# Performance work log

Measured on AMD Instinct MI355X. Metric: run time of the kernel, lower is better.

The kernel has to match this reference:

```python
import jax, jax.numpy as jnp
import numpy as np

N_NODES = 100000
N_EDGES = 1600000
IN_CH = 128
HID = 64
N_CLASSES = 16
N_GRAPHS = 64


def setup_inputs() -> dict:
    key = jax.random.key(0)
    ks = jax.random.split(key, 10)
    x = jax.random.normal(ks[0], (N_NODES, IN_CH), dtype=jnp.float32)
    edge_index = jax.random.randint(ks[1], (2, N_EDGES), 0, N_NODES, dtype=jnp.int64)
    edge_weight = jax.random.uniform(ks[2], (N_EDGES,), dtype=jnp.float32)
    batch = jnp.sort(jax.random.randint(ks[3], (N_NODES,), 0, N_GRAPHS, dtype=jnp.int64))
    s1 = 1.0 / np.sqrt(IN_CH)
    s2 = 1.0 / np.sqrt(HID)
    W1 = jax.random.uniform(ks[4], (IN_CH, HID), jnp.float32, -s1, s1)
    b1 = jnp.zeros((HID,), jnp.float32)
    W2 = jax.random.uniform(ks[5], (HID, HID), jnp.float32, -s2, s2)
    b2 = jnp.zeros((HID,), jnp.float32)
    Wl = jax.random.uniform(ks[6], (HID, N_CLASSES), jnp.float32, -s2, s2)
    bl = jax.random.uniform(ks[7], (N_CLASSES,), jnp.float32, -s2, s2)
    return {"x": x, "edge_index": edge_index, "edge_weight": edge_weight,
            "batch": batch, "W1": W1, "b1": b1, "W2": W2, "b2": b2,
            "Wl": Wl, "bl": bl}


def _gcn_conv(x, src, dst, ew, W, b, n_nodes):
    # PyG GCNConv: h = x @ W; symmetric normalization with self-loops;
    # out[dst] += norm * h[src]; out += bias.
    deg = jax.ops.segment_sum(ew, dst, num_segments=n_nodes)
    deg_inv_sqrt = jnp.where(deg > 0, jax.lax.rsqrt(jnp.maximum(deg, 1e-30)), 0.0)
    norm = deg_inv_sqrt[src] * ew * deg_inv_sqrt[dst]  # [E']
    h = x @ W                                          # [N, out]
    msg = h[src] * norm[:, None]                       # [E', out] gather
    out = jax.ops.segment_sum(msg, dst, num_segments=n_nodes)  # scatter-add
    return out + b


def reference(x, edge_index, edge_weight, batch, W1, b1, W2, b2, Wl, bl):
    n = x.shape[0]
    # add self loops once (weight 1.0), shared by both conv layers
    loop = jnp.arange(n, dtype=edge_index.dtype)
    src = jnp.concatenate([edge_index[0], loop])
    dst = jnp.concatenate([edge_index[1], loop])
    ew = jnp.concatenate([edge_weight, jnp.ones((n,), edge_weight.dtype)])

    h = jax.nn.relu(_gcn_conv(x, src, dst, ew, W1, b1, n))
    h = jax.nn.relu(_gcn_conv(h, src, dst, ew, W2, b2, n))

    # global_mean_pool over graphs
    sums = jax.ops.segment_sum(h, batch, num_segments=N_GRAPHS)  # [G, HID]
    cnt = jax.ops.segment_sum(jnp.ones((n,), h.dtype), batch, num_segments=N_GRAPHS)
    pooled = sums / jnp.maximum(cnt, 1.0)[:, None]

    return pooled @ Wl + bl
```

## Files before the change

### kernel.cpp

```cpp
#include <hip/hip_runtime.h>
#include <hip/hip_fp16.h>

#define N_NODES   100000
#define N_EDGES   1600000
#define IN_CH     128
#define HID       64
#define N_CLASSES 16
#define N_GRAPHS  64

#define BK_SH     9
#define BK_NODES  512
#define NB        ((N_NODES + BK_NODES - 1) / BK_NODES)
#define BK_CAP    10240
#define CH_EDGES  4096
#define EPT       16
#define NCH       ((N_EDGES + CH_EDGES - 1) / CH_EDGES)
#define AGG_NPW   8

typedef __attribute__((ext_vector_type(8))) short bf16x8;
typedef __attribute__((ext_vector_type(4))) float f32x4;

__device__ __forceinline__ unsigned short f2bf(float f) {
    unsigned u = __float_as_uint(f);
    u += 0x7fffu + ((u >> 16) & 1u);
    return (unsigned short)(u >> 16);
}
__device__ __forceinline__ float4 bf4(uint2 v) {
    float4 o;
    o.x = __uint_as_float(v.x << 16);
    o.y = __uint_as_float(v.x & 0xffff0000u);
    o.z = __uint_as_float(v.y << 16);
    o.w = __uint_as_float(v.y & 0xffff0000u);
    return o;
}
__device__ __forceinline__ float dec_ew(unsigned v) {
    return __half2float(__ushort_as_half((unsigned short)(v >> 17)));
}

__global__ void k_init(int* __restrict__ bcursor, float* __restrict__ pooled,
                       float* __restrict__ cnt) {
    int i = blockIdx.x * 256 + threadIdx.x;
    if (i < NB) bcursor[i] = i * BK_CAP;
    if (i < N_GRAPHS * HID) pooled[i] = 0.0f;
    if (i < N_GRAPHS) cnt[i] = 0.0f;
}

__global__ void k_binscatter(const int* __restrict__ src, const int* __restrict__ dst,
                             const float* __restrict__ ew, int* __restrict__ bcursor,
                             int2* __restrict__ bedges) {
    __shared__ int  hist[NB];
    __shared__ int  offs[NB];
    __shared__ int  gbase[NB];
    __shared__ int  sc[256];
    __shared__ int2 stage[CH_EDGES];
    __shared__ int  dest[CH_EDGES];
    const int t = threadIdx.x;
    const int base = blockIdx.x * CH_EDGES;
    const int nloc = min(CH_EDGES, N_EDGES - base);

    for (int i = t; i < NB; i += 256) hist[i] = 0;
    __syncthreads();

    int myb[EPT], myr[EPT], myp[EPT]; float myw[EPT];
#pragma unroll
    for (int j = 0; j < EPT; ++j) {
        int i = base + j * 256 + t;
        if (i < N_EDGES) {
            int s = src[i], d = dst[i];
            int b = d >> BK_SH;
            myb[j] = b;
            myr[j] = atomicAdd(&hist[b], 1);
            myp[j] = s | ((d & (BK_NODES - 1)) << 17);
            myw[j] = ew[i];
        } else {
            myb[j] = -1;
        }
    }
    __syncthreads();

    int v = (t < NB) ? hist[t] : 0;
    sc[t] = v;
    __syncthreads();
    for (int off = 1; off < 256; off <<= 1) {
        int a = (t >= off) ? sc[t - off] : 0;
        __syncthreads();
        sc[t] += a;
        __syncthreads();
    }
    if (t < NB) {
        offs[t] = sc[t] - v;
        gbase[t] = (v > 0) ? atomicAdd(&bcursor[t], v) : 0;
    }
    __syncthreads();

#pragma unroll
    for (int j = 0; j < EPT; ++j) {
        if (myb[j] >= 0) {
            int p = offs[myb[j]] + myr[j];
            stage[p] = make_int2(myp[j], __float_as_int(myw[j]));
            dest[p] = gbase[myb[j]] + myr[j];
        }
    }
    __syncthreads();

    for (int i = t; i < nloc; i += 256)
        bedges[dest[i]] = stage[i];
}

__global__ __launch_bounds__(256) void k_build(const int* __restrict__ bcursor,
                                               const int2* __restrict__ bedges,
                                               int2* __restrict__ rowse,
                                               float* __restrict__ dis,
                                               unsigned* __restrict__ csr) {
    __shared__ int2  eds[BK_CAP];
    __shared__ int   cnt[BK_NODES];
    __shared__ float dsum[BK_NODES];
    __shared__ int   cur[BK_NODES];
    __shared__ int   sc[256];
    const int b = blockIdx.x;
    const int t = threadIdx.x;
    const int beg = b * BK_CAP, end = bcursor[b];
    const int n = end - beg;

    for (int i = t; i < BK_NODES; i += 256) { cnt[i] = 0; dsum[i] = 0.0f; }
    __syncthreads();

    for (int i = t; i < n; i += 256) {
        int2 e = bedges[beg + i];
        eds[i] = e;
        int dl = ((unsigned)e.x) >> 17;
        atomicAdd(&cnt[dl], 1);
        atomicAdd(&dsum[dl], __int_as_float(e.y));
    }
    __syncthreads();

    int a0 = cnt[2 * t], a1 = cnt[2 * t + 1];
    int pair = a0 + a1;
    sc[t] = pair;
    __syncthreads();
    for (int off = 1; off < 256; off <<= 1) {
        int a = (t >= off) ? sc[t - off] : 0;
        __syncthreads();
        sc[t] += a;
        __syncthreads();
    }
    int excl = sc[t] - pair;
    cur[2 * t] = excl;
    cur[2 * t + 1] = excl + a0;
    {
        int n0 = b * BK_NODES + 2 * t;
        if (n0 < N_NODES) {
            rowse[n0] = make_int2(beg + excl, beg + excl + a0);
            dis[n0] = rsqrtf(1.0f + dsum[2 * t]);
        }
        int n1 = n0 + 1;
        if (n1 < N_NODES) {
            rowse[n1] = make_int2(beg + excl + a0, beg + excl + a0 + a1);
            dis[n1] = rsqrtf(1.0f + dsum[2 * t + 1]);
        }
    }
    __syncthreads();

    for (int i = t; i < n; i += 256) {
        int2 e = eds[i];
        int dl = ((unsigned)e.x) >> 17;
        int s = e.x & 0x1FFFF;
        unsigned short w16 = __half_as_ushort(__float2half(__int_as_float(e.y)));
        int pos = beg + atomicAdd(&cur[dl], 1);
        csr[pos] = (unsigned)s | ((unsigned)w16 << 17);
    }
}

template <int K>
__global__ __launch_bounds__(256) void k_gemm(const float* __restrict__ x,
                                              const float* __restrict__ W,
                                              const float* __restrict__ dis,
                                              unsigned short* __restrict__ hb) {
    constexpr int AS = K + 8;
    __shared__ unsigned short a_s[64 * AS];
    __shared__ unsigned short wt[64 * AS];
    const int t    = threadIdx.x;
    const int lane = t & 63;
    const int wave = t >> 6;
    const int m    = lane & 15;
    const int quad = lane >> 4;
    const int rowbase = blockIdx.x * 64;

    constexpr int CPR = K / 8;
    for (int c = t; c < 64 * CPR; c += 256) {
        int row = c / CPR, cc = c % CPR;
        int gr = rowbase + row;
        float4 v0, v1;
        if (gr < N_NODES) {
            v0 = *(const float4*)&x[(long)gr * K + cc * 8];
            v1 = *(const float4*)&x[(long)gr * K + cc * 8 + 4];
        } else {
            v0 = make_float4(0.f, 0.f, 0.f, 0.f); v1 = v0;
        }
        uint4 p;
        p.x = f2bf(v0.x) | ((unsigned)f2bf(v0.y) << 16);
        p.y = f2bf(v0.z) | ((unsigned)f2bf(v0.w) << 16);
        p.z = f2bf(v1.x) | ((unsigned)f2bf(v1.y) << 16);
        p.w = f2bf(v1.z) | ((unsigned)f2bf(v1.w) << 16);
        *(uint4*)&a_s[row * AS + cc * 8] = p;
    }
    for (int idx = t; idx < K * 64; idx += 256) {
        int k = idx >> 6, n = idx & 63;
        wt[n * AS + k] = f2bf(W[idx]);
    }
    __syncthreads();

    bf16x8 bfrag[4][K / 32];
#pragma unroll
    for (int nt = 0; nt < 4; ++nt)
#pragma unroll
        for (int ks = 0; ks < K / 32; ++ks)
            bfrag[nt][ks] = *(const bf16x8*)&wt[(nt * 16 + m) * AS + ks * 32 + quad * 8];

    f32x4 acc[4];
#pragma unroll
    for (int nt = 0; nt < 4; ++nt) acc[nt] = (f32x4){0.f, 0.f, 0.f, 0.f};

#pragma unroll
    for (int ks = 0; ks < K / 32; ++ks) {
        bf16x8 af = *(const bf16x8*)&a_s[(wave * 16 + m) * AS + ks * 32 + quad * 8];
#pragma unroll
        for (int nt = 0; nt < 4; ++nt)
            acc[nt] = __builtin_amdgcn_mfma_f32_16x16x32_bf16(af, bfrag[nt][ks],
                                                              acc[nt], 0, 0, 0);
    }

#pragma unroll
    for (int i = 0; i < 4; ++i) {
        int gr = rowbase + wave * 16 + quad * 4 + i;
        if (gr < N_NODES) {
            float dsc = dis[gr];
#pragma unroll
            for (int nt = 0; nt < 4; ++nt)
                hb[(long)gr * HID + nt * 16 + m] = f2bf(dsc * acc[nt][i]);
        }
    }
}

__global__ void k_aggregate(const int2* __restrict__ rowse, const unsigned* __restrict__ csr,
                            const uint2* __restrict__ hb, const float* __restrict__ dis,
                            const float* __restrict__ b, float4* __restrict__ out4) {
    const int tid  = threadIdx.x;
    const int lane = tid & 63;
    const int g    = lane >> 4;
    const int c4   = lane & 15;
    const int nodebase = (blockIdx.x * 4 + (tid >> 6)) * AGG_NPW;
    const float4 bb = ((const float4*)b)[c4];

    if (nodebase >= N_NODES) return;

    int2 rs = rowse[nodebase];
    uint2 hsr = hb[nodebase * 16 + c4];

    for (int j = 0; j < AGG_NPW; ++j) {
        const int node = nodebase + j;
        if (node >= N_NODES) return;

        const int2 rs_c = rs;
        const float4 hs = bf4(hsr);
        if (j + 1 < AGG_NPW && node + 1 < N_NODES) {
            rs  = rowse[node + 1];
            hsr = hb[(node + 1) * 16 + c4];
        }

        float4 acc;
        if (g == 0) { acc = hs; }
        else        { acc.x = 0.f; acc.y = 0.f; acc.z = 0.f; acc.w = 0.f; }

        int p = rs_c.x;
        const int end = rs_c.y;

        unsigned d0, d1, d2, d3;
        if (p + 16 <= end) {
            d0 = csr[p + g];     d1 = csr[p + 4 + g];
            d2 = csr[p + 8 + g]; d3 = csr[p + 12 + g];
        }
        while (p + 16 <= end) {
            const unsigned e0 = d0, e1 = d1, e2 = d2, e3 = d3;
            const int pn = p + 16;
            if (pn + 16 <= end) {
                d0 = csr[pn + g];     d1 = csr[pn + 4 + g];
                d2 = csr[pn + 8 + g]; d3 = csr[pn + 12 + g];
            }
            float4 v0 = bf4(hb[(e0 & 0x1FFFF) * 16 + c4]);
            float4 v1 = bf4(hb[(e1 & 0x1FFFF) * 16 + c4]);
            float4 v2 = bf4(hb[(e2 & 0x1FFFF) * 16 + c4]);
            float4 v3 = bf4(hb[(e3 & 0x1FFFF) * 16 + c4]);
            float w0 = dec_ew(e0), w1 = dec_ew(e1);
            float w2 = dec_ew(e2), w3 = dec_ew(e3);
            acc.x += w0 * v0.x; acc.y += w0 * v0.y; acc.z += w0 * v0.z; acc.w += w0 * v0.w;
            acc.x += w1 * v1.x; acc.y += w1 * v1.y; acc.z += w1 * v1.z; acc.w += w1 * v1.w;
            acc.x += w2 * v2.x; acc.y += w2 * v2.y; acc.z += w2 * v2.z; acc.w += w2 * v2.w;
            acc.x += w3 * v3.x; acc.y += w3 * v3.y; acc.z += w3 * v3.z; acc.w += w3 * v3.w;
            p = pn;
        }
        if (p < end) {
            int i0 = p + g, i1 = p + 4 + g, i2 = p + 8 + g, i3 = p + 12 + g;
            unsigned e0 = csr[min(i0, end - 1)];
            unsigned e1 = csr[min(i1, end - 1)];
            unsigned e2 = csr[min(i2, end - 1)];
            unsigned e3 = csr[min(i3, end - 1)];
            float4 v0 = bf4(hb[(e0 & 0x1FFFF) * 16 + c4]);
            float4 v1 = bf4(hb[(e1 & 0x1FFFF) * 16 + c4]);
            float4 v2 = bf4(hb[(e2 & 0x1FFFF) * 16 + c4]);
            float4 v3 = bf4(hb[(e3 & 0x1FFFF) * 16 + c4]);
            float w0 = (i0 < end) ? dec_ew(e0) : 0.0f;
            float w1 = (i1 < end) ? dec_ew(e1) : 0.0f;
            float w2 = (i2 < end) ? dec_ew(e2) : 0.0f;
            float w3 = (i3 < end) ? dec_ew(e3) : 0.0f;
            acc.x += w0 * v0.x; acc.y += w0 * v0.y; acc.z += w0 * v0.z; acc.w += w0 * v0.w;
            acc.x += w1 * v1.x; acc.y += w1 * v1.y; acc.z += w1 * v1.z; acc.w += w1 * v1.w;
            acc.x += w2 * v2.x; acc.y += w2 * v2.y; acc.z += w2 * v2.z; acc.w += w2 * v2.w;
            acc.x += w3 * v3.x; acc.y += w3 * v3.y; acc.z += w3 * v3.z; acc.w += w3 * v3.w;
        }

        acc.x += __shfl_xor(acc.x, 16); acc.y += __shfl_xor(acc.y, 16);
        acc.z += __shfl_xor(acc.z, 16); acc.w += __shfl_xor(acc.w, 16);
        acc.x += __shfl_xor(acc.x, 32); acc.y += __shfl_xor(acc.y, 32);
        acc.z += __shfl_xor(acc.z, 32); acc.w += __shfl_xor(acc.w, 32);

        if (g == 0) {
            const float dd = dis[node];
            float4 o;
            o.x = fmaxf(dd * acc.x + bb.x, 0.0f);
            o.y = fmaxf(dd * acc.y + bb.y, 0.0f);
            o.z = fmaxf(dd * acc.z + bb.z, 0.0f);
            o.w = fmaxf(dd * acc.w + bb.w, 0.0f);
            out4[node * 16 + c4] = o;
        }
    }
}

#define POOL_NPB 256
__global__ __launch_bounds__(1024) void k_pool(const float* __restrict__ agg,
                                               const int* __restrict__ batch,
                                               float* __restrict__ pooled,
                                               float* __restrict__ cnt) {
    __shared__ float psh[N_GRAPHS * HID];
    __shared__ float csh[N_GRAPHS];
    const int tid = threadIdx.x;
    const int c = tid & 63;
    const int w = tid >> 6;
    const int nodebase = blockIdx.x * POOL_NPB + w * 16;

    for (int i = tid; i < N_GRAPHS * HID; i += 1024) psh[i] = 0.f;
    if (tid < N_GRAPHS) csh[tid] = 0.f;
    __syncthreads();

    int curg = -1; float accv = 0.f, cntacc = 0.f;
    for (int j = 0; j < 16; ++j) {
        int node = nodebase + j;
        if (node >= N_NODES) break;
        int g = batch[node];
        float v = agg[node * HID + c];
        if (g != curg) {
            if (curg >= 0) {
                atomicAdd(&psh[curg * HID + c], accv);
                if (c == 0) atomicAdd(&csh[curg], cntacc);
            }
            curg = g; accv = 0.f; cntacc = 0.f;
        }
        accv += v; cntacc += 1.f;
    }
    if (curg >= 0) {
        atomicAdd(&psh[curg * HID + c], accv);
        if (c == 0) atomicAdd(&csh[curg], cntacc);
    }
    __syncthreads();

    for (int i = tid; i < N_GRAPHS * HID; i += 1024) {
        if (csh[i >> 6] > 0.f) atomicAdd(&pooled[i], psh[i]);
    }
    if (tid < N_GRAPHS && csh[tid] > 0.f) atomicAdd(&cnt[tid], csh[tid]);
}

__global__ void k_out(const float* __restrict__ pooled, const float* __restrict__ cnt,
                      const float* __restrict__ Wl, const float* __restrict__ bl,
                      float* __restrict__ out) {
    int tid = threadIdx.x;
    int g = tid >> 4, k = tid & 15;
    float inv = 1.0f / fmaxf(cnt[g], 1.0f);
    float acc = 0.f;
#pragma unroll
    for (int h = 0; h < HID; ++h) acc += pooled[g * HID + h] * Wl[h * N_CLASSES + k];
    out[g * N_CLASSES + k] = acc * inv + bl[k];
}

extern "C" void kernel_launch(void* const* d_in, const int* in_sizes, int n_in,
                              void* d_out, int out_size, void* d_ws, size_t ws_size,
                              hipStream_t stream) {
    const float* x     = (const float*)d_in[0];
    const int*   ei    = (const int*)d_in[1];
    const float* ew    = (const float*)d_in[2];
    const int*   batch = (const int*)d_in[3];
    const float* W1    = (const float*)d_in[4];
    const float* b1    = (const float*)d_in[5];
    const float* W2    = (const float*)d_in[6];
    const float* b2    = (const float*)d_in[7];
    const float* Wl    = (const float*)d_in[8];
    const float* bl    = (const float*)d_in[9];

    const int* srcv = ei;
    const int* dstv = ei + N_EDGES;

    char* wsb = (char*)d_ws;
    float*          dis    = (float*)wsb;              wsb += 100352 * 4;
    int2*           rowse  = (int2*)wsb;               wsb += 100352 * 8;
    int*            bcursor= (int*)wsb;                wsb += 256 * 4;
    unsigned*       csr    = (unsigned*)wsb;           wsb += (size_t)NB * BK_CAP * 4;
    unsigned short* hb     = (unsigned short*)wsb;     wsb += N_NODES * HID * 2;
    float*          agg    = (float*)wsb;              wsb += N_NODES * HID * 4;
    float*          pooled = (float*)wsb;              wsb += N_GRAPHS * HID * 4;
    float*          cnt    = (float*)wsb;              wsb += N_GRAPHS * 4;
    float*          out    = (float*)d_out;
    int2*           bedges = (int2*)agg;

    k_init<<<16, 256, 0, stream>>>(bcursor, pooled, cnt);
    k_binscatter<<<NCH, 256, 0, stream>>>(srcv, dstv, ew, bcursor, bedges);
    k_build<<<NB, 256, 0, stream>>>(bcursor, bedges, rowse, dis, csr);

    const int agg_blocks = (N_NODES + 4 * AGG_NPW - 1) / (4 * AGG_NPW);

    k_gemm<IN_CH><<<(N_NODES + 63) / 64, 256, 0, stream>>>(x, W1, dis, hb);
    k_aggregate<<<agg_blocks, 256, 0, stream>>>(rowse, csr, (const uint2*)hb,
                                                dis, b1, (float4*)agg);
    k_gemm<HID><<<(N_NODES + 63) / 64, 256, 0, stream>>>(agg, W2, dis, hb);
    k_aggregate<<<agg_blocks, 256, 0, stream>>>(rowse, csr, (const uint2*)hb,
                                                dis, b2, (float4*)agg);

    k_pool<<<(N_NODES + POOL_NPB - 1) / POOL_NPB, 1024, 0, stream>>>(
        agg, batch, pooled, cnt);
    k_out<<<1, N_GRAPHS * N_CLASSES, 0, stream>>>(pooled, cnt, Wl, bl, out);
}
```

Measured before the change: 269.8 us.

## Simplify binscatter to direct writes and pass layer-1 output as bf16

The edge binning kernel drops the shared-memory prefix scan and staging buffer. It now uses smaller chunks with higher occupancy and writes each edge straight to its global bucket slot. The first aggregation now emits bf16 activations, and a new bf16-input GEMM reads them, halving intermediate traffic between layer 1 and layer 2. In exchange, the scatter writes are less coalesced, there are twice as many bcursor atomics, and rounding layer-1 outputs to bf16 adds precision loss.

```diff
diff --git a/kernel.cpp b/kernel.cpp
--- a/kernel.cpp
+++ b/kernel.cpp
@@ -12,8 +12,8 @@
 #define BK_NODES  512
 #define NB        ((N_NODES + BK_NODES - 1) / BK_NODES)
 #define BK_CAP    10240
-#define CH_EDGES  4096
-#define EPT       16
+#define CH_EDGES  2048
+#define EPT       8
 #define NCH       ((N_EDGES + CH_EDGES - 1) / CH_EDGES)
 #define AGG_NPW   8
 
@@ -45,18 +45,14 @@
     if (i < N_GRAPHS) cnt[i] = 0.0f;
 }
 
-__global__ void k_binscatter(const int* __restrict__ src, const int* __restrict__ dst,
-                             const float* __restrict__ ew, int* __restrict__ bcursor,
-                             int2* __restrict__ bedges) {
-    __shared__ int  hist[NB];
-    __shared__ int  offs[NB];
-    __shared__ int  gbase[NB];
-    __shared__ int  sc[256];
-    __shared__ int2 stage[CH_EDGES];
-    __shared__ int  dest[CH_EDGES];
+__global__ __launch_bounds__(256, 8) void k_binscatter(
+        const int* __restrict__ src, const int* __restrict__ dst,
+        const float* __restrict__ ew, int* __restrict__ bcursor,
+        int2* __restrict__ bedges) {
+    __shared__ int hist[NB];
+    __shared__ int gbase[NB];
     const int t = threadIdx.x;
     const int base = blockIdx.x * CH_EDGES;
-    const int nloc = min(CH_EDGES, N_EDGES - base);
 
     for (int i = t; i < NB; i += 256) hist[i] = 0;
     __syncthreads();
@@ -78,33 +74,18 @@
     }
     __syncthreads();
 
-    int v = (t < NB) ? hist[t] : 0;
-    sc[t] = v;
-    __syncthreads();
-    for (int off = 1; off < 256; off <<= 1) {
-        int a = (t >= off) ? sc[t - off] : 0;
-        __syncthreads();
-        sc[t] += a;
-        __syncthreads();
-    }
     if (t < NB) {
-        offs[t] = sc[t] - v;
+        int v = hist[t];
         gbase[t] = (v > 0) ? atomicAdd(&bcursor[t], v) : 0;
     }
     __syncthreads();
 
 #pragma unroll
     for (int j = 0; j < EPT; ++j) {
-        if (myb[j] >= 0) {
-            int p = offs[myb[j]] + myr[j];
-            stage[p] = make_int2(myp[j], __float_as_int(myw[j]));
-            dest[p] = gbase[myb[j]] + myr[j];
-        }
-    }
-    __syncthreads();
-
-    for (int i = t; i < nloc; i += 256)
-        bedges[dest[i]] = stage[i];
+        if (myb[j] >= 0)
+            bedges[gbase[myb[j]] + myr[j]] =
+                make_int2(myp[j], __float_as_int(myw[j]));
+    }
 }
 
 __global__ __launch_bounds__(256) void k_build(const int* __restrict__ bcursor,
@@ -242,9 +223,71 @@
     }
 }
 
+__global__ __launch_bounds__(256) void k_gemm2(const unsigned short* __restrict__ xb,
+                                               const float* __restrict__ W,
+                                               const float* __restrict__ dis,
+                                               unsigned short* __restrict__ hb) {
+    constexpr int K = HID;
+    constexpr int AS = K + 8;
+    __shared__ unsigned short a_s[64 * AS];
+    __shared__ unsigned short wt[64 * AS];
+    const int t    = threadIdx.x;
+    const int lane = t & 63;
+    const int wave = t >> 6;
+    const int m    = lane & 15;
+    const int quad = lane >> 4;
+    const int rowbase = blockIdx.x * 64;
+
+    for (int c = t; c < 64 * 8; c += 256) {
+        int row = c >> 3, cc = c & 7;
+        int gr = rowbase + row;
+        uint4 p = (gr < N_NODES) ? *(const uint4*)&xb[(long)gr * K + cc * 8]
+                                 : make_uint4(0, 0, 0, 0);
+        *(uint4*)&a_s[row * AS + cc * 8] = p;
+    }
+    for (int idx = t; idx < K * 64; idx += 256) {
+        int k = idx >> 6, n = idx & 63;
+        wt[n * AS + k] = f2bf(W[idx]);
+    }
+    __syncthreads();
+
+    bf16x8 bfrag[4][K / 32];
+#pragma unroll
+    for (int nt = 0; nt < 4; ++nt)
+#pragma unroll
+        for (int ks = 0; ks < K / 32; ++ks)
+            bfrag[nt][ks] = *(const bf16x8*)&wt[(nt * 16 + m) * AS + ks * 32 + quad * 8];
+
+    f32x4 acc[4];
+#pragma unroll
+    for (int nt = 0; nt < 4; ++nt) acc[nt] = (f32x4){0.f, 0.f, 0.f, 0.f};
+
+#pragma unroll
+    for (int ks = 0; ks < K / 32; ++ks) {
+        bf16x8 af = *(const bf16x8*)&a_s[(wave * 16 + m) * AS + ks * 32 + quad * 8];
+#pragma unroll
+        for (int nt = 0; nt < 4; ++nt)
+            acc[nt] = __builtin_amdgcn_mfma_f32_16x16x32_bf16(af, bfrag[nt][ks],
+                                                              acc[nt], 0, 0, 0);
+    }
+
+#pragma unroll
+    for (int i = 0; i < 4; ++i) {
+        int gr = rowbase + wave * 16 + quad * 4 + i;
+        if (gr < N_NODES) {
+            float dsc = dis[gr];
+#pragma unroll
+            for (int nt = 0; nt < 4; ++nt)
+                hb[(long)gr * HID + nt * 16 + m] = f2bf(dsc * acc[nt][i]);
+        }
+    }
+}
+
+template <bool OUT_BF16>
 __global__ void k_aggregate(const int2* __restrict__ rowse, const unsigned* __restrict__ csr,
                             const uint2* __restrict__ hb, const float* __restrict__ dis,
-                            const float* __restrict__ b, float4* __restrict__ out4) {
+                            const float* __restrict__ b, float4* __restrict__ out4,
+                            ushort4* __restrict__ outb) {
     const int tid  = threadIdx.x;
     const int lane = tid & 63;
     const int g    = lane >> 4;
@@ -331,7 +374,14 @@
             o.y = fmaxf(dd * acc.y + bb.y, 0.0f);
             o.z = fmaxf(dd * acc.z + bb.z, 0.0f);
             o.w = fmaxf(dd * acc.w + bb.w, 0.0f);
-            out4[node * 16 + c4] = o;
+            if (OUT_BF16) {
+                ushort4 ob;
+                ob.x = f2bf(o.x); ob.y = f2bf(o.y);
+                ob.z = f2bf(o.z); ob.w = f2bf(o.w);
+                outb[node * 16 + c4] = ob;
+            } else {
+                out4[node * 16 + c4] = o;
+            }
         }
     }
 }
@@ -414,6 +464,7 @@
     int*            bcursor= (int*)wsb;                wsb += 256 * 4;
     unsigned*       csr    = (unsigned*)wsb;           wsb += (size_t)NB * BK_CAP * 4;
     unsigned short* hb     = (unsigned short*)wsb;     wsb += N_NODES * HID * 2;
+    unsigned short* hbn    = (unsigned short*)wsb;     wsb += N_NODES * HID * 2;
     float*          agg    = (float*)wsb;              wsb += N_NODES * HID * 4;
     float*          pooled = (float*)wsb;              wsb += N_GRAPHS * HID * 4;
     float*          cnt    = (float*)wsb;              wsb += N_GRAPHS * 4;
@@ -427,11 +478,11 @@
     const int agg_blocks = (N_NODES + 4 * AGG_NPW - 1) / (4 * AGG_NPW);
 
     k_gemm<IN_CH><<<(N_NODES + 63) / 64, 256, 0, stream>>>(x, W1, dis, hb);
-    k_aggregate<<<agg_blocks, 256, 0, stream>>>(rowse, csr, (const uint2*)hb,
-                                                dis, b1, (float4*)agg);
-    k_gemm<HID><<<(N_NODES + 63) / 64, 256, 0, stream>>>(agg, W2, dis, hb);
-    k_aggregate<<<agg_blocks, 256, 0, stream>>>(rowse, csr, (const uint2*)hb,
-                                                dis, b2, (float4*)agg);
+    k_aggregate<true><<<agg_blocks, 256, 0, stream>>>(rowse, csr, (const uint2*)hb,
+                                                      dis, b1, nullptr, (ushort4*)hbn);
+    k_gemm2<<<(N_NODES + 63) / 64, 256, 0, stream>>>(hbn, W2, dis, hb);
+    k_aggregate<false><<<agg_blocks, 256, 0, stream>>>(rowse, csr, (const uint2*)hb,
+                                                       dis, b2, (float4*)agg, nullptr);
 
     k_pool<<<(N_NODES + POOL_NPB - 1) / POOL_NPB, 1024, 0, stream>>>(
         agg, batch, pooled, cnt);
```

Result: slower. 281.1 us (+4.2%).
